# Kernel optimization log

Measured on AMD Instinct MI355X. Metric: run time of the kernel, lower is better.

## Reference

```python
import jax, jax.numpy as jnp
import numpy as np

RES = 100          # resolution
ITERS = 1000       # lowfid solver iterations
INIT_MIN = 0.01    # conductivity floor (init_min)
BATCH = 32
HIDDEN = [128, 256, 512]


def conductivity_original(pores, res):
    """Coarse 5x5 pore map -> base conductivity on the fine res x res grid.
    pore present (1) -> low conductivity (0), solid (0) -> conductivity 1."""
    B = pores.shape[0]
    grid = 1.0 - pores.reshape(B, 5, 5)
    f = res // 5
    return jnp.repeat(jnp.repeat(grid, f, axis=1), f, axis=2)  # (B, res, res)


def mlp_forward(x, params):
    n = len(params)
    for i, (W, b) in enumerate(params):
        x = x @ W + b
        if i < n - 1:
            x = jax.nn.relu(x)
    return x


def lowfid_solve(k):
    """1000-iteration Jacobi relaxation of variable-coefficient steady heat
    equation with T=1 on top edge, T=0 on bottom edge, insulated sides.
    Returns effective conductivity kappa per sample, shape (B,)."""
    B, res, _ = k.shape
    # face conductivities (arithmetic mean of adjacent cells, edge-padded)
    kp = jnp.pad(k, ((0, 0), (1, 1), (1, 1)), mode='edge')
    kN = 0.5 * (k + kp[:, :-2, 1:-1])
    kS = 0.5 * (k + kp[:, 2:, 1:-1])
    kW = 0.5 * (k + kp[:, 1:-1, :-2])
    kE = 0.5 * (k + kp[:, 1:-1, 2:])
    denom = kN + kS + kW + kE + 1e-12

    def step(T, _):
        Tp = jnp.pad(T, ((0, 0), (0, 0), (1, 1)), mode='edge')        # side Neumann
        Tp = jnp.pad(Tp, ((0, 0), (1, 1), (0, 0)))                    # top/bottom Dirichlet
        Tp = Tp.at[:, 0, :].set(1.0)                                   # T=1 at top, T=0 at bottom
        T_new = (kN * Tp[:, :-2, 1:-1] + kS * Tp[:, 2:, 1:-1]
                 + kW * Tp[:, 1:-1, :-2] + kE * Tp[:, 1:-1, 2:]) / denom
        return T_new, None

    T0 = jnp.broadcast_to(jnp.linspace(1.0, 0.0, res)[None, :, None], (B, res, res))
    T, _ = jax.lax.scan(step, T0, None, length=ITERS)
    # heat flux through top boundary; domain size 1, dT = 1 -> kappa = mean flux
    kappa = jnp.mean(2.0 * res * k[:, 0, :] * (1.0 - T[:, 0, :]), axis=1)
    return kappa


def setup_inputs() -> dict:
    key = jax.random.key(0)
    ks = jax.random.split(key, 10)
    pores = (jax.random.uniform(ks[0], (BATCH, 25)) > 0.5).astype(jnp.float32)
    sizes = [25] + HIDDEN + [RES * RES]
    inp = {"pores": pores}
    for i in range(len(sizes) - 1):
        fan_in = sizes[i]
        W = jax.random.normal(ks[1 + 2 * i], (sizes[i], sizes[i + 1]), jnp.float32) * np.sqrt(2.0 / fan_in)
        b = jnp.zeros((sizes[i + 1],), jnp.float32)
        inp[f"W{i + 1}"] = W
        inp[f"b{i + 1}"] = b
    return inp


def reference(pores, W1, b1, W2, b2, W3, b3, W4, b4):
    params = [(W1, b1), (W2, b2), (W3, b3), (W4, b4)]
    B = pores.shape[0]
    gen = mlp_forward(pores.reshape(B, 25), params).reshape(B, RES, RES)
    cond = gen + conductivity_original(pores, RES)   # learn_residual
    cond = jnp.maximum(cond, INIT_MIN)               # relu clamp to init_min
    kappa = lowfid_solve(cond)
    return kappa, cond
```

## Files before the change

### kernel.cpp

```cpp
#include <hip/hip_runtime.h>
#include <hip/hip_bf16.h>

#define RES   100
#define ITERS 1000
#define SLOTP 128

typedef float vf2 __attribute__((ext_vector_type(2)));

__global__ __launch_bounds__(256) void mlp123(const float* __restrict__ pores,
                                              const float* __restrict__ W1, const float* __restrict__ b1,
                                              const float* __restrict__ W2, const float* __restrict__ b2,
                                              const float* __restrict__ W3, const float* __restrict__ b3,
                                              float* __restrict__ x3out) {
    __shared__ float x1[128];
    __shared__ float x2[256];
    const int s = blockIdx.x, tid = threadIdx.x;

    if (tid < 128) {
        float acc = b1[tid];
#pragma unroll
        for (int k = 0; k < 25; ++k)
            acc = fmaf(pores[s * 25 + k], W1[k * 128 + tid], acc);
        x1[tid] = fmaxf(acc, 0.0f);
    }
    __syncthreads();

    {
        float acc = b2[tid];
#pragma unroll 8
        for (int k = 0; k < 128; ++k)
            acc = fmaf(x1[k], W2[k * 256 + tid], acc);
        x2[tid] = fmaxf(acc, 0.0f);
    }
    __syncthreads();

    {
        float a0 = b3[tid], a1 = b3[tid + 256];
#pragma unroll 8
        for (int k = 0; k < 256; ++k) {
            float xv = x2[k];
            a0 = fmaf(xv, W3[k * 512 + tid],       a0);
            a1 = fmaf(xv, W3[k * 512 + tid + 256], a1);
        }
        x3out[s * 512 + tid]       = fmaxf(a0, 0.0f);
        x3out[s * 512 + tid + 256] = fmaxf(a1, 0.0f);
    }
}

__global__ __launch_bounds__(256) void fc4_fused(const float* __restrict__ X3,
                                                 const float* __restrict__ W4,
                                                 const float* __restrict__ b4,
                                                 const float* __restrict__ pores,
                                                 float* __restrict__ cond) {
    const int j = blockIdx.x * 256 + threadIdx.x;
    if (j >= RES * RES) return;
    const int bg = blockIdx.y;
    const float* x = X3 + bg * 8 * 512;

    float acc[8];
    float bj = b4[j];
#pragma unroll
    for (int b = 0; b < 8; ++b) acc[b] = bj;

    for (int k0 = 0; k0 < 512; k0 += 8) {
        float w[8];
#pragma unroll
        for (int u = 0; u < 8; ++u)
            w[u] = W4[(k0 + u) * (RES * RES) + j];
#pragma unroll
        for (int u = 0; u < 8; ++u) {
#pragma unroll
            for (int b = 0; b < 8; ++b)
                acc[b] = fmaf(x[b * 512 + k0 + u], w[u], acc[b]);
        }
    }

    const int row = j / RES, col = j % RES;
    const int p = (row / 20) * 5 + (col / 20);
#pragma unroll
    for (int b = 0; b < 8; ++b) {
        int bb = bg * 8 + b;
        float base = 1.0f - pores[bb * 25 + p];
        cond[bb * RES * RES + j] = fmaxf(acc[b] + base, 0.01f);
    }
}

__device__ __forceinline__ float dpp_shr1(float old_v, float src) {
    return __int_as_float(__builtin_amdgcn_update_dpp(
        __float_as_int(old_v), __float_as_int(src), 0x138, 0xf, 0xf, false));
}
__device__ __forceinline__ float dpp_shl1(float old_v, float src) {
    return __int_as_float(__builtin_amdgcn_update_dpp(
        __float_as_int(old_v), __float_as_int(src), 0x130, 0xf, 0xf, false));
}

template<int R>
__device__ __forceinline__ void jstep(const vf2* __restrict__ nptr, const vf2* __restrict__ sptr,
                                      vf2* __restrict__ topptr, vf2* __restrict__ botptr,
                                      const vf2* wN, const vf2* wS,
                                      const vf2* wA, const vf2* wB,
                                      const vf2* Tin, vf2* Tout, bool fix49) {
    vf2 nval = *nptr;
    vf2 sval = *sptr;
#pragma unroll
    for (int r = 0; r < R; ++r) {
        vf2 nb = (r == 0)     ? nval : Tin[r - 1];
        vf2 sb = (r == R - 1) ? sval : Tin[r + 1];
        float lo = Tin[r].x, hi = Tin[r].y;
        float wlo = dpp_shr1(lo, hi);
        float ehi = dpp_shl1(hi, lo);
        ehi = fix49 ? hi : ehi;
        vf2 P1; P1.x = wlo; P1.y = ehi;
        vf2 TS; TS.x = hi;  TS.y = lo;
        Tout[r] = wN[r] * nb + wS[r] * sb + wA[r] * P1 + wB[r] * TS;
    }
    *topptr = Tout[0];
    *botptr = Tout[R - 1];
}

__global__ __launch_bounds__(1024) void jacobi(const float* __restrict__ cond,
                                               float* __restrict__ kappa_out) {
    __shared__ float kst[RES * RES];
    __shared__ float SA[34 * SLOTP];
    __shared__ float SB[34 * SLOTP];

    const int b   = blockIdx.x;
    const int tid = threadIdx.x;

    for (int i = tid; i < RES * RES; i += 1024)
        kst[i] = cond[b * RES * RES + i];
    if (tid < SLOTP) {
        SA[32 * SLOTP + tid] = 1.0f;  SA[33 * SLOTP + tid] = 0.0f;
        SB[32 * SLOTP + tid] = 1.0f;  SB[33 * SLOTP + tid] = 0.0f;
    }
    __syncthreads();

    const int w    = tid >> 6;
    const int lane = tid & 63;
    const int R    = (w < 4) ? 7 : 6;
    const int r0   = (w < 4) ? 7 * w : 28 + 6 * (w - 4);
    const int c0   = min(2 * lane, 98), c1 = c0 + 1;
    const int lane2 = 2 * lane;
    const bool fix49 = (lane == 49);

    vf2 wN[7], wS[7], wA[7], wB[7], T0[7], T1[7];

#pragma unroll
    for (int r = 0; r < 7; ++r) {
        if (r < R) {
            int i   = r0 + r;
            int in_ = i ? i - 1 : 0;
            int is_ = (i < RES - 1) ? i + 1 : RES - 1;
            int jw  = c0 ? c0 - 1 : 0;
            int je  = (c1 < RES - 1) ? c1 + 1 : RES - 1;
            float kc0 = kst[i * RES + c0], kc1 = kst[i * RES + c1];
            float kn0 = 0.5f * (kc0 + kst[in_ * RES + c0]);
            float kn1 = 0.5f * (kc1 + kst[in_ * RES + c1]);
            float ks0 = 0.5f * (kc0 + kst[is_ * RES + c0]);
            float ks1 = 0.5f * (kc1 + kst[is_ * RES + c1]);
            float kw0 = 0.5f * (kc0 + kst[i * RES + jw]);
            float kw1 = 0.5f * (kc1 + kc0);
            float ke0 = 0.5f * (kc0 + kc1);
            float ke1 = 0.5f * (kc1 + kst[i * RES + je]);
            float inv0 = 1.0f / (kn0 + ks0 + kw0 + ke0 + 1e-12f);
            float inv1 = 1.0f / (kn1 + ks1 + kw1 + ke1 + 1e-12f);
            wN[r].x = kn0 * inv0;  wN[r].y = kn1 * inv1;
            wS[r].x = ks0 * inv0;  wS[r].y = ks1 * inv1;
            wA[r].x = kw0 * inv0;  wA[r].y = ke1 * inv1;
            wB[r].x = ke0 * inv0;  wB[r].y = kw1 * inv1;
            float v = 1.0f - (float)i * (1.0f / (RES - 1));
            T0[r].x = v;  T0[r].y = v;
        }
    }

    vf2 bot0 = (w < 4) ? T0[6] : T0[5];
    *(vf2*)(SA + (2 * w) * SLOTP + lane2)     = T0[0];
    *(vf2*)(SA + (2 * w + 1) * SLOTP + lane2) = bot0;
    __syncthreads();

    const int nslot = (w == 0)  ? 32 : (2 * w - 1);
    const int sslot = (w == 15) ? 33 : (2 * w + 2);
    const int topsl = 2 * w;

    const vf2* SAn = (const vf2*)(SA + nslot * SLOTP + lane2);
    const vf2* SAs = (const vf2*)(SA + sslot * SLOTP + lane2);
    const vf2* SBn = (const vf2*)(SB + nslot * SLOTP + lane2);
    const vf2* SBs = (const vf2*)(SB + sslot * SLOTP + lane2);
    vf2* SAtop = (vf2*)(SA + topsl * SLOTP + lane2);
    vf2* SAbot = (vf2*)(SA + (topsl + 1) * SLOTP + lane2);
    vf2* SBtop = (vf2*)(SB + topsl * SLOTP + lane2);
    vf2* SBbot = (vf2*)(SB + (topsl + 1) * SLOTP + lane2);

    for (int it = 0; it < ITERS / 2; ++it) {
        if (w < 4) jstep<7>(SAn, SAs, SBtop, SBbot, wN, wS, wA, wB, T0, T1, fix49);
        else       jstep<6>(SAn, SAs, SBtop, SBbot, wN, wS, wA, wB, T0, T1, fix49);
        __syncthreads();
        if (w < 4) jstep<7>(SBn, SBs, SAtop, SAbot, wN, wS, wA, wB, T1, T0, fix49);
        else       jstep<6>(SBn, SBs, SAtop, SAbot, wN, wS, wA, wB, T1, T0, fix49);
        __syncthreads();
    }

    if (w == 0) {
        float s = 0.0f;
        if (lane < 50)
            s = kst[c0] * (1.0f - T0[0].x) + kst[c1] * (1.0f - T0[0].y);
        for (int off = 32; off; off >>= 1)
            s += __shfl_down(s, off);
        if (lane == 0) kappa_out[b] = 2.0f * s;
    }
}

extern "C" void kernel_launch(void* const* d_in, const int* in_sizes, int n_in,
                              void* d_out, int out_size, void* d_ws, size_t ws_size,
                              hipStream_t stream) {
    (void)in_sizes; (void)n_in; (void)out_size; (void)ws_size;
    const float* pores = (const float*)d_in[0];
    const float* W1 = (const float*)d_in[1];
    const float* b1 = (const float*)d_in[2];
    const float* W2 = (const float*)d_in[3];
    const float* b2 = (const float*)d_in[4];
    const float* W3 = (const float*)d_in[5];
    const float* b3 = (const float*)d_in[6];
    const float* W4 = (const float*)d_in[7];
    const float* b4 = (const float*)d_in[8];

    float* x3 = (float*)d_ws;

    float* kappa = (float*)d_out;
    float* cond  = kappa + 32;

    mlp123<<<32, 256, 0, stream>>>(pores, W1, b1, W2, b2, W3, b3, x3);
    fc4_fused<<<dim3(40, 4), 256, 0, stream>>>(x3, W4, b4, pores, cond);
    jacobi<<<32, 1024, 0, stream>>>(cond, kappa);
}
```

Before: 648.1 us.

## Transpose Jacobi grid mapping so lanes span rows and waves own columns

Each wave now owns a block of columns and each lane holds two adjacent rows, so the north/south neighbours come from DPP lane shifts and the east/west halos go through shared memory. The Dirichlet top/bottom boundaries are folded into precomputed per-cell coefficients (a constant term C and zeroed weights), which removes the boundary slots and the per-step lane-49 select. The closing flux reduction is reworked to take one value per wave through a small shared array. The per-iteration instruction count stays roughly the same: the old select is traded for an extra constant add.

Result: faster. 545.1 us (-15.9%).

```diff
diff --git a/kernel.cpp b/kernel.cpp
--- a/kernel.cpp
+++ b/kernel.cpp
@@ -85,34 +85,37 @@
     }
 }
 
-__device__ __forceinline__ float dpp_shr1(float old_v, float src) {
+__device__ __forceinline__ float dpp_shr1_z(float src) {
     return __int_as_float(__builtin_amdgcn_update_dpp(
-        __float_as_int(old_v), __float_as_int(src), 0x138, 0xf, 0xf, false));
-}
-__device__ __forceinline__ float dpp_shl1(float old_v, float src) {
+        0, __float_as_int(src), 0x138, 0xf, 0xf, true));
+}
+__device__ __forceinline__ float dpp_shl1_z(float src) {
     return __int_as_float(__builtin_amdgcn_update_dpp(
-        __float_as_int(old_v), __float_as_int(src), 0x130, 0xf, 0xf, false));
+        0, __float_as_int(src), 0x130, 0xf, 0xf, true));
+}
+
+__device__ __forceinline__ vf2 jrowT(vf2 wv, vf2 ev, vf2 c,
+                                     vf2 wWr, vf2 wEr, vf2 wPr, vf2 wTr, vf2 Cr) {
+    float nlo = dpp_shr1_z(c.y);
+    float shi = dpp_shl1_z(c.x);
+    vf2 P;  P.x  = nlo; P.y  = shi;
+    vf2 TS; TS.x = c.y; TS.y = c.x;
+    return Cr + wPr * P + wTr * TS + wWr * wv + wEr * ev;
 }
 
 template<int R>
-__device__ __forceinline__ void jstep(const vf2* __restrict__ nptr, const vf2* __restrict__ sptr,
-                                      vf2* __restrict__ topptr, vf2* __restrict__ botptr,
-                                      const vf2* wN, const vf2* wS,
-                                      const vf2* wA, const vf2* wB,
-                                      const vf2* Tin, vf2* Tout, bool fix49) {
-    vf2 nval = *nptr;
-    vf2 sval = *sptr;
+__device__ __forceinline__ void jstepT(const vf2* __restrict__ wptr, const vf2* __restrict__ eptr,
+                                       vf2* __restrict__ topptr, vf2* __restrict__ botptr,
+                                       const vf2* wW, const vf2* wE,
+                                       const vf2* wP, const vf2* wT, const vf2* C,
+                                       const vf2* Tin, vf2* Tout) {
+    vf2 wval = *wptr;
+    vf2 eval = *eptr;
 #pragma unroll
     for (int r = 0; r < R; ++r) {
-        vf2 nb = (r == 0)     ? nval : Tin[r - 1];
-        vf2 sb = (r == R - 1) ? sval : Tin[r + 1];
-        float lo = Tin[r].x, hi = Tin[r].y;
-        float wlo = dpp_shr1(lo, hi);
-        float ehi = dpp_shl1(hi, lo);
-        ehi = fix49 ? hi : ehi;
-        vf2 P1; P1.x = wlo; P1.y = ehi;
-        vf2 TS; TS.x = hi;  TS.y = lo;
-        Tout[r] = wN[r] * nb + wS[r] * sb + wA[r] * P1 + wB[r] * TS;
+        vf2 wv = (r == 0)     ? wval : Tin[r - 1];
+        vf2 ev = (r == R - 1) ? eval : Tin[r + 1];
+        Tout[r] = jrowT(wv, ev, Tin[r], wW[r], wE[r], wP[r], wT[r], C[r]);
     }
     *topptr = Tout[0];
     *botptr = Tout[R - 1];
@@ -121,55 +124,55 @@
 __global__ __launch_bounds__(1024) void jacobi(const float* __restrict__ cond,
                                                float* __restrict__ kappa_out) {
     __shared__ float kst[RES * RES];
-    __shared__ float SA[34 * SLOTP];
-    __shared__ float SB[34 * SLOTP];
+    __shared__ float SA[32 * SLOTP];
+    __shared__ float SB[32 * SLOTP];
+    __shared__ float red[16];
 
     const int b   = blockIdx.x;
     const int tid = threadIdx.x;
 
     for (int i = tid; i < RES * RES; i += 1024)
         kst[i] = cond[b * RES * RES + i];
-    if (tid < SLOTP) {
-        SA[32 * SLOTP + tid] = 1.0f;  SA[33 * SLOTP + tid] = 0.0f;
-        SB[32 * SLOTP + tid] = 1.0f;  SB[33 * SLOTP + tid] = 0.0f;
-    }
     __syncthreads();
 
     const int w    = tid >> 6;
     const int lane = tid & 63;
     const int R    = (w < 4) ? 7 : 6;
-    const int r0   = (w < 4) ? 7 * w : 28 + 6 * (w - 4);
-    const int c0   = min(2 * lane, 98), c1 = c0 + 1;
+    const int c0   = (w < 4) ? 7 * w : 28 + 6 * (w - 4);
+    const int l    = min(lane, 49);
+    const int i0   = 2 * l, i1 = 2 * l + 1;
     const int lane2 = 2 * lane;
-    const bool fix49 = (lane == 49);
-
-    vf2 wN[7], wS[7], wA[7], wB[7], T0[7], T1[7];
+
+    vf2 wW[7], wE[7], wP[7], wT[7], C[7], T0[7], T1[7];
 
 #pragma unroll
     for (int r = 0; r < 7; ++r) {
         if (r < R) {
-            int i   = r0 + r;
-            int in_ = i ? i - 1 : 0;
-            int is_ = (i < RES - 1) ? i + 1 : RES - 1;
-            int jw  = c0 ? c0 - 1 : 0;
-            int je  = (c1 < RES - 1) ? c1 + 1 : RES - 1;
-            float kc0 = kst[i * RES + c0], kc1 = kst[i * RES + c1];
-            float kn0 = 0.5f * (kc0 + kst[in_ * RES + c0]);
-            float kn1 = 0.5f * (kc1 + kst[in_ * RES + c1]);
-            float ks0 = 0.5f * (kc0 + kst[is_ * RES + c0]);
-            float ks1 = 0.5f * (kc1 + kst[is_ * RES + c1]);
-            float kw0 = 0.5f * (kc0 + kst[i * RES + jw]);
-            float kw1 = 0.5f * (kc1 + kc0);
-            float ke0 = 0.5f * (kc0 + kc1);
-            float ke1 = 0.5f * (kc1 + kst[i * RES + je]);
+            int c  = c0 + r;
+            int in_ = i0 ? i0 - 1 : 0;
+            int is_ = (i1 < RES - 1) ? i1 + 1 : RES - 1;
+            int jw  = c ? c - 1 : 0;
+            int je  = (c < RES - 1) ? c + 1 : RES - 1;
+            float kc0 = kst[i0 * RES + c], kc1 = kst[i1 * RES + c];
+            float kn0 = 0.5f * (kc0 + kst[in_ * RES + c]);
+            float ks0 = 0.5f * (kc0 + kc1);
+            float kw0 = 0.5f * (kc0 + kst[i0 * RES + jw]);
+            float ke0 = 0.5f * (kc0 + kst[i0 * RES + je]);
+            float kn1 = 0.5f * (kc1 + kc0);
+            float ks1 = 0.5f * (kc1 + kst[is_ * RES + c]);
+            float kw1 = 0.5f * (kc1 + kst[i1 * RES + jw]);
+            float ke1 = 0.5f * (kc1 + kst[i1 * RES + je]);
             float inv0 = 1.0f / (kn0 + ks0 + kw0 + ke0 + 1e-12f);
             float inv1 = 1.0f / (kn1 + ks1 + kw1 + ke1 + 1e-12f);
-            wN[r].x = kn0 * inv0;  wN[r].y = kn1 * inv1;
-            wS[r].x = ks0 * inv0;  wS[r].y = ks1 * inv1;
-            wA[r].x = kw0 * inv0;  wA[r].y = ke1 * inv1;
-            wB[r].x = ke0 * inv0;  wB[r].y = kw1 * inv1;
-            float v = 1.0f - (float)i * (1.0f / (RES - 1));
-            T0[r].x = v;  T0[r].y = v;
+            wW[r].x = kw0 * inv0;  wW[r].y = kw1 * inv1;
+            wE[r].x = ke0 * inv0;  wE[r].y = ke1 * inv1;
+            wP[r].x = (l == 0)  ? 0.0f : kn0 * inv0;
+            wP[r].y = (l >= 49) ? 0.0f : ks1 * inv1;
+            wT[r].x = ks0 * inv0;  wT[r].y = kn1 * inv1;
+            C[r].x = (l == 0) ? kn0 * inv0 : 0.0f;
+            C[r].y = 0.0f;
+            T0[r].x = 1.0f - (float)i0 * (1.0f / (RES - 1));
+            T0[r].y = 1.0f - (float)i1 * (1.0f / (RES - 1));
         }
     }
 
@@ -178,35 +181,41 @@
     *(vf2*)(SA + (2 * w + 1) * SLOTP + lane2) = bot0;
     __syncthreads();
 
-    const int nslot = (w == 0)  ? 32 : (2 * w - 1);
-    const int sslot = (w == 15) ? 33 : (2 * w + 2);
+    const int wslot = (w == 0)  ? 0  : (2 * w - 1);
+    const int eslot = (w == 15) ? 31 : (2 * w + 2);
     const int topsl = 2 * w;
 
-    const vf2* SAn = (const vf2*)(SA + nslot * SLOTP + lane2);
-    const vf2* SAs = (const vf2*)(SA + sslot * SLOTP + lane2);
-    const vf2* SBn = (const vf2*)(SB + nslot * SLOTP + lane2);
-    const vf2* SBs = (const vf2*)(SB + sslot * SLOTP + lane2);
+    const vf2* SAw = (const vf2*)(SA + wslot * SLOTP + lane2);
+    const vf2* SAe = (const vf2*)(SA + eslot * SLOTP + lane2);
+    const vf2* SBw = (const vf2*)(SB + wslot * SLOTP + lane2);
+    const vf2* SBe = (const vf2*)(SB + eslot * SLOTP + lane2);
     vf2* SAtop = (vf2*)(SA + topsl * SLOTP + lane2);
     vf2* SAbot = (vf2*)(SA + (topsl + 1) * SLOTP + lane2);
     vf2* SBtop = (vf2*)(SB + topsl * SLOTP + lane2);
     vf2* SBbot = (vf2*)(SB + (topsl + 1) * SLOTP + lane2);
 
     for (int it = 0; it < ITERS / 2; ++it) {
-        if (w < 4) jstep<7>(SAn, SAs, SBtop, SBbot, wN, wS, wA, wB, T0, T1, fix49);
-        else       jstep<6>(SAn, SAs, SBtop, SBbot, wN, wS, wA, wB, T0, T1, fix49);
+        if (w < 4) jstepT<7>(SAw, SAe, SBtop, SBbot, wW, wE, wP, wT, C, T0, T1);
+        else       jstepT<6>(SAw, SAe, SBtop, SBbot, wW, wE, wP, wT, C, T0, T1);
         __syncthreads();
-        if (w < 4) jstep<7>(SBn, SBs, SAtop, SAbot, wN, wS, wA, wB, T1, T0, fix49);
-        else       jstep<6>(SBn, SBs, SAtop, SAbot, wN, wS, wA, wB, T1, T0, fix49);
+        if (w < 4) jstepT<7>(SBw, SBe, SAtop, SAbot, wW, wE, wP, wT, C, T1, T0);
+        else       jstepT<6>(SBw, SBe, SAtop, SAbot, wW, wE, wP, wT, C, T1, T0);
         __syncthreads();
     }
 
-    if (w == 0) {
+    if (lane == 0) {
+        float part = 0.0f;
+#pragma unroll
+        for (int r = 0; r < 7; ++r)
+            if (r < R) part = fmaf(kst[c0 + r], 1.0f - T0[r].x, part);
+        red[w] = part;
+    }
+    __syncthreads();
+    if (tid == 0) {
         float s = 0.0f;
-        if (lane < 50)
-            s = kst[c0] * (1.0f - T0[0].x) + kst[c1] * (1.0f - T0[0].y);
-        for (int off = 32; off; off >>= 1)
-            s += __shfl_down(s, off);
-        if (lane == 0) kappa_out[b] = 2.0f * s;
+#pragma unroll
+        for (int i = 0; i < 16; ++i) s += red[i];
+        kappa_out[b] = 2.0f * s;
     }
 }
 
```
